# Kernel optimization log

Hardware: AMD Instinct MI355X
Metric: run time of the kernel (lower is better)

## Reference

```python
import jax, jax.numpy as jnp
import numpy as np

B, D, W, H = 512, 128, 256, 256  # batch, drive_num, window_size, hidden_size


def setup_inputs() -> dict:
    key = jax.random.key(0)
    k = jax.random.split(key, 7)
    x = jax.random.normal(k[0], (B, D, W), jnp.float32)
    # encode_attn: Linear(window_size + 2*hidden_size, 1)
    attn_w = jax.random.normal(k[1], (W + 2 * H,), jnp.float32) * 0.02
    attn_b = jax.random.normal(k[2], (), jnp.float32) * 0.02
    # single-layer LSTM, input_size=D, hidden_size=H; PyTorch gate order i,f,g,o
    W_ih = jax.random.normal(k[3], (4 * H, D), jnp.float32) * 0.05
    W_hh = jax.random.normal(k[4], (4 * H, H), jnp.float32) * 0.05
    b_ih = jax.random.normal(k[5], (4 * H,), jnp.float32) * 0.05
    b_hh = jax.random.normal(k[6], (4 * H,), jnp.float32) * 0.05
    return {"x": x, "attn_w": attn_w, "attn_b": attn_b,
            "W_ih": W_ih, "W_hh": W_hh, "b_ih": b_ih, "b_hh": b_hh}


def reference(x, attn_w, attn_b, W_ih, W_hh, b_ih, b_hh):
    # x: [B, D, W]
    h_dim = W_hh.shape[1]
    w_h = attn_w[:h_dim]           # weight on repeated hidden state
    w_c = attn_w[h_dim:2 * h_dim]  # weight on repeated cell state
    w_x = attn_w[2 * h_dim:]       # weight on full input row (constant over t)
    # precompute input contribution to attention logits: [B, D]
    e_x = jnp.einsum('bdw,w->bd', x, w_x) + attn_b
    x_steps = jnp.moveaxis(x, 2, 0)  # [W, B, D]

    def step(carry, x_t):
        h, c = carry  # [B, H] each
        # attention logit: h/c terms broadcast over drive dim
        e = e_x + (h @ w_h + c @ w_c)[:, None]  # [B, D]
        a = jax.nn.softmax(e, axis=-1)
        x_hat = a * x_t  # [B, D]
        gates = x_hat @ W_ih.T + b_ih + h @ W_hh.T + b_hh  # [B, 4H]
        i, f, g, o = jnp.split(gates, 4, axis=-1)
        c_new = jax.nn.sigmoid(f) * c + jax.nn.sigmoid(i) * jnp.tanh(g)
        h_new = jax.nn.sigmoid(o) * jnp.tanh(c_new)
        return (h_new, c_new), h_new

    bsz = x.shape[0]
    h0 = jnp.zeros((bsz, h_dim), x.dtype)
    c0 = jnp.zeros((bsz, h_dim), x.dtype)
    _, hs = jax.lax.scan(step, (h0, c0), x_steps)  # hs: [W, B, H]
    return jnp.transpose(hs, (1, 0, 2))  # [B, W, H] == hidden_states[:, 1:]
```

## Files before the change

kernel.cpp:

```cpp
#include <hip/hip_runtime.h>
#include <cstdint>

#define NB 512
#define ND 128
#define NW 256
#define NH 256
#define PGRP 32
#define QGRP 8

typedef _Float16 f16;
typedef _Float16 h8 __attribute__((ext_vector_type(8)));
typedef float f32x4 __attribute__((ext_vector_type(4)));
typedef unsigned long long u64;

#define FLAG_DONE 0x0101010101010101ull

__device__ __forceinline__ float sigm(float v){ return 1.f/(1.f+__expf(-v)); }
__device__ __forceinline__ float tanh_fast(float v){
  v = fminf(fmaxf(v,-15.f),15.f);
  float e = __expf(2.f*v);
  return (e-1.f)/(e+1.f);
}

__global__ __launch_bounds__(128) void attn_kernel(
    const float* __restrict__ x, const float* __restrict__ attn_w,
    const float* __restrict__ attn_b, float* __restrict__ a_buf)
{
    __shared__ float wx[NW];
    __shared__ float sred[2];
    const int b = blockIdx.x;
    const int d = threadIdx.x;

    wx[d]       = attn_w[2 * NH + d];
    wx[d + 128] = attn_w[2 * NH + d + 128];
    __syncthreads();

    const float4* xr = (const float4*)(x + ((size_t)b * ND + d) * NW);
    float acc = 0.f;
    #pragma unroll 8
    for (int w4 = 0; w4 < NW / 4; ++w4) {
        float4 v = xr[w4];
        acc += v.x * wx[w4*4+0] + v.y * wx[w4*4+1]
             + v.z * wx[w4*4+2] + v.w * wx[w4*4+3];
    }
    float e = acc + attn_b[0];

    float mx = e;
    #pragma unroll
    for (int o = 32; o > 0; o >>= 1) mx = fmaxf(mx, __shfl_xor(mx, o));
    if ((d & 63) == 0) sred[d >> 6] = mx;
    __syncthreads();
    mx = fmaxf(sred[0], sred[1]);
    __syncthreads();

    float p = __expf(e - mx);
    float s = p;
    #pragma unroll
    for (int o = 32; o > 0; o >>= 1) s += __shfl_xor(s, o);
    if ((d & 63) == 0) sred[d >> 6] = s;
    __syncthreads();
    s = sred[0] + sred[1];

    a_buf[(size_t)b * ND + d] = p / s;
}

__global__ __launch_bounds__(512) void pack_kernel(
    const float* __restrict__ W_ih, const float* __restrict__ W_hh,
    const float* __restrict__ b_ih, const float* __restrict__ b_hh,
    f16* __restrict__ Wfrag, float* __restrict__ bias)
{
    int flat = blockIdx.x * 512 + threadIdx.x;
    int l    = flat & 63;
    int kt   = (flat >> 6) % 12;
    int wq   = (flat >> 6) / 12;
    int col16 = l & 15, kb = l >> 4;
    int hcol = (wq >> 3) * 32 + (wq & 7) * 4 + (col16 >> 2);
    int gate = col16 & 3;
    int n    = gate * 256 + hcol;
    int k0   = kt * 32 + kb * 8;

    f16 tmp[8];
    #pragma unroll
    for (int e = 0; e < 8; ++e) {
        int k = k0 + e;
        float v = (k < NH) ? W_hh[(size_t)n * NH + k]
                           : W_ih[(size_t)n * ND + (k - NH)];
        tmp[e] = (f16)v;
    }
    *(h8*)(Wfrag + (size_t)flat * 8) = *(const h8*)tmp;

    if (flat < 1024) bias[flat] = b_ih[flat] + b_hh[flat];
}

__global__ __launch_bounds__(512) void init_kernel(unsigned* __restrict__ flags)
{
    flags[blockIdx.x * 512 + threadIdx.x] = 0u;
}

__global__ __launch_bounds__(512, 2) void lstm_kernel(
    const float* __restrict__ x, const float* __restrict__ a_buf,
    const float* __restrict__ bias, const f16* __restrict__ Wfrag,
    f16* __restrict__ hx, u64* __restrict__ flags,
    float* __restrict__ out)
{
    __shared__ __align__(16) unsigned char A16[16 * 768];
    __shared__ float scr[8][272];

    const int tid = threadIdx.x;
    const int w = tid >> 6, l = tid & 63;
    const int p = blockIdx.x & 31, q = blockIdx.x >> 5;

    h8 bfrag[12];
    {
        const h8* wsrc = (const h8*)Wfrag + ((q * 8 + w) * 12) * 64 + l;
        #pragma unroll
        for (int kt = 0; kt < 12; ++kt) bfrag[kt] = wsrc[kt * 64];
    }

    const int m = l >> 2, hh = l & 3;
    const int jcol = q * 32 + w * 4 + hh;
    float bias4[4];
    #pragma unroll
    for (int g = 0; g < 4; ++g) bias4[g] = bias[g * 256 + jcol];
    float cstate = 0.f;

    float areg[8];
    const float* xbase = nullptr;
    const int xrow = tid >> 4, xdc = tid & 15;
    if (tid < 256) {
        int b = p * 16 + xrow;
        #pragma unroll
        for (int e = 0; e < 8; ++e) areg[e] = a_buf[b * ND + xdc * 8 + e];
        xbase = x + ((size_t)b * ND + xdc * 8) * NW;
    }
    const int r2 = tid >> 5, kc = tid & 31;
    const int arow = l & 15, akb = l >> 4;

    float4 xq[8];

    {
        int byte = r2 * 768 + kc * 16;
        byte ^= (r2 & 7) << 4;
        h8 z = {};
        *(h8*)(A16 + byte) = z;
    }
    if (tid < 256) {
        #pragma unroll
        for (int e = 0; e < 8; ++e)
            xq[e] = *(const float4*)(xbase + (size_t)e * NW);
        f16 xv[8];
        #pragma unroll
        for (int e = 0; e < 8; ++e) {
            float xf = xq[e].x;
            xq[e] = make_float4(xq[e].y, xq[e].z, xq[e].w, xq[e].x);
            xv[e] = (f16)(xf * areg[e]);
        }
        int byte = xrow * 768 + 512 + xdc * 16;
        byte ^= (xrow & 7) << 4;
        *(h8*)(A16 + byte) = *(const h8*)xv;
    }

    for (int t = 0; t < NW; ++t) {
        if (t > 0 && tid == 0) {
            while (__hip_atomic_load(&flags[(t - 1) * PGRP + p],
                                     __ATOMIC_RELAXED, __HIP_MEMORY_SCOPE_AGENT)
                   != FLAG_DONE) {}
        }
        __syncthreads();

        f32x4 acc = {0.f, 0.f, 0.f, 0.f};
        if (t > 0) {
            const u64* hrow = (const u64*)
                (hx + ((size_t)((t - 1) & 1) * NB + p * 16 + r2) * NH);
            u64 d0 = __hip_atomic_load(hrow + kc * 2 + 0,
                    __ATOMIC_RELAXED, __HIP_MEMORY_SCOPE_AGENT);
            u64 d1 = __hip_atomic_load(hrow + kc * 2 + 1,
                    __ATOMIC_RELAXED, __HIP_MEMORY_SCOPE_AGENT);
            #pragma unroll
            for (int kt = 8; kt < 12; ++kt) {
                int byte = arow * 768 + kt * 64 + akb * 16;
                byte ^= (arow & 7) << 4;
                h8 afrag = *(const h8*)(A16 + byte);
                acc = __builtin_amdgcn_mfma_f32_16x16x32_f16(afrag, bfrag[kt], acc, 0, 0, 0);
            }
            int byte = r2 * 768 + kc * 16;
            byte ^= (r2 & 7) << 4;
            ((u64*)(A16 + byte))[0] = d0;
            ((u64*)(A16 + byte))[1] = d1;
        } else {
            #pragma unroll
            for (int kt = 8; kt < 12; ++kt) {
                int byte = arow * 768 + kt * 64 + akb * 16;
                byte ^= (arow & 7) << 4;
                h8 afrag = *(const h8*)(A16 + byte);
                acc = __builtin_amdgcn_mfma_f32_16x16x32_f16(afrag, bfrag[kt], acc, 0, 0, 0);
            }
        }
        __syncthreads();

        #pragma unroll
        for (int kt = 0; kt < 8; ++kt) {
            int byte = arow * 768 + kt * 64 + akb * 16;
            byte ^= (arow & 7) << 4;
            h8 afrag = *(const h8*)(A16 + byte);
            acc = __builtin_amdgcn_mfma_f32_16x16x32_f16(afrag, bfrag[kt], acc, 0, 0, 0);
        }

        float hn;
        {
            float* sw = &scr[w][0];
            int col = l & 15, rb = (l >> 4) * 4;
            sw[(rb + 0) * 17 + col] = acc[0];
            sw[(rb + 1) * 17 + col] = acc[1];
            sw[(rb + 2) * 17 + col] = acc[2];
            sw[(rb + 3) * 17 + col] = acc[3];
            asm volatile("s_waitcnt lgkmcnt(0)" ::: "memory");
            float G0 = sw[m * 17 + hh * 4 + 0] + bias4[0];
            float G1 = sw[m * 17 + hh * 4 + 1] + bias4[1];
            float G2 = sw[m * 17 + hh * 4 + 2] + bias4[2];
            float G3 = sw[m * 17 + hh * 4 + 3] + bias4[3];
            float ig = sigm(G0), fg = sigm(G1);
            float gg = tanh_fast(G2), og = sigm(G3);
            cstate = fg * cstate + ig * gg;
            hn = og * tanh_fast(cstate);

            f16 hf = (f16)hn;
            unsigned short hb = __builtin_bit_cast(unsigned short, hf);
            int other = __shfl_xor((int)hb, 1);
            if (!(l & 1)) {
                unsigned val = (unsigned)hb | ((unsigned)(unsigned short)other << 16);
                unsigned* dst = (unsigned*)((unsigned short*)hx
                                + ((size_t)(t & 1) * NB + p * 16 + m) * NH + jcol);
                __hip_atomic_store(dst, val, __ATOMIC_RELAXED, __HIP_MEMORY_SCOPE_AGENT);
            }
        }
        asm volatile("s_waitcnt vmcnt(0)" ::: "memory");
        __syncthreads();

        if (tid == 0) {
            unsigned char* fb = ((unsigned char*)&flags[t * PGRP + p]) + q;
            __hip_atomic_store(fb, (unsigned char)1,
                               __ATOMIC_RELAXED, __HIP_MEMORY_SCOPE_AGENT);
        }

        out[((size_t)(p * 16 + m) * NW + t) * NH + jcol] = hn;

        if (tid < 256 && t + 1 < NW) {
            if (((t + 1) & 3) == 0) {
                #pragma unroll
                for (int e = 0; e < 8; ++e)
                    xq[e] = *(const float4*)(xbase + (size_t)e * NW + (t + 1));
            }
            f16 xv[8];
            #pragma unroll
            for (int e = 0; e < 8; ++e) {
                float xf = xq[e].x;
                xq[e] = make_float4(xq[e].y, xq[e].z, xq[e].w, xq[e].x);
                xv[e] = (f16)(xf * areg[e]);
            }
            int byte = xrow * 768 + 512 + xdc * 16;
            byte ^= (xrow & 7) << 4;
            *(h8*)(A16 + byte) = *(const h8*)xv;
        }
    }
}

extern "C" void kernel_launch(void* const* d_in, const int* in_sizes, int n_in,
                              void* d_out, int out_size, void* d_ws, size_t ws_size,
                              hipStream_t stream) {
    (void)in_sizes; (void)n_in; (void)out_size;

    const float* x      = (const float*)d_in[0];
    const float* attn_w = (const float*)d_in[1];
    const float* attn_b = (const float*)d_in[2];
    const float* W_ih   = (const float*)d_in[3];
    const float* W_hh   = (const float*)d_in[4];
    const float* b_ih   = (const float*)d_in[5];
    const float* b_hh   = (const float*)d_in[6];
    float* out = (float*)d_out;

    char* ws = (char*)d_ws;
    float* a_buf = (float*)ws;
    float* bias  = (float*)(ws + 262144);
    f16*   Wfrag = (f16*)(ws + 266240);
    f16*   hx    = (f16*)(ws + 1052672);
    u64*   flags = (u64*)(ws + 1576960);
    if (ws_size < (size_t)1642496) return;

    attn_kernel<<<NB, 128, 0, stream>>>(x, attn_w, attn_b, a_buf);
    pack_kernel<<<96, 512, 0, stream>>>(W_ih, W_hh, b_ih, b_hh, Wfrag, bias);
    init_kernel<<<32, 512, 0, stream>>>((unsigned*)flags);
    lstm_kernel<<<PGRP * QGRP, 512, 0, stream>>>(x, a_buf, bias, Wfrag, hx, flags, out);
}
```

Baseline: 797.8 us.

## Replace per-step flag barrier with sentinel-poisoned hidden-state ring buffer polling

Removes the per-timestep flag word and the single-thread spin plus block barrier. Consumers now poll the hidden-state data directly until no fp16 infinity sentinel remains. Producers re-poison a slot three steps ahead in an 8-slot ring, and the x-input MFMAs are issued before the wait. This cuts one global round trip and a barrier from the cross-block dependency chain on each step. In exchange every thread spins on global loads, and correctness depends on the sentinel value never occurring as a real h value (fp16 +inf) and on the slot-reuse distance.

Result: slower. 818.7 us (+2.6%).

```diff
diff --git a/kernel.cpp b/kernel.cpp
--- a/kernel.cpp
+++ b/kernel.cpp
@@ -7,13 +7,14 @@
 #define NH 256
 #define PGRP 32
 #define QGRP 8
+#define SLOTS 8
+#define SENT32 0x7C007C00u
+#define SENT64 0x7C007C007C007C00ull
 
 typedef _Float16 f16;
 typedef _Float16 h8 __attribute__((ext_vector_type(8)));
 typedef float f32x4 __attribute__((ext_vector_type(4)));
 typedef unsigned long long u64;
-
-#define FLAG_DONE 0x0101010101010101ull
 
 __device__ __forceinline__ float sigm(float v){ return 1.f/(1.f+__expf(-v)); }
 __device__ __forceinline__ float tanh_fast(float v){
@@ -92,16 +93,16 @@
     if (flat < 1024) bias[flat] = b_ih[flat] + b_hh[flat];
 }
 
-__global__ __launch_bounds__(512) void init_kernel(unsigned* __restrict__ flags)
-{
-    flags[blockIdx.x * 512 + threadIdx.x] = 0u;
+__global__ __launch_bounds__(512) void poison_kernel(uint4* __restrict__ hx4)
+{
+    uint4 v = {SENT32, SENT32, SENT32, SENT32};
+    hx4[(size_t)blockIdx.x * 512 + threadIdx.x] = v;
 }
 
 __global__ __launch_bounds__(512, 2) void lstm_kernel(
     const float* __restrict__ x, const float* __restrict__ a_buf,
     const float* __restrict__ bias, const f16* __restrict__ Wfrag,
-    f16* __restrict__ hx, u64* __restrict__ flags,
-    float* __restrict__ out)
+    f16* __restrict__ hx, float* __restrict__ out)
 {
     __shared__ __align__(16) unsigned char A16[16 * 768];
     __shared__ float scr[8][272];
@@ -135,6 +136,7 @@
     }
     const int r2 = tid >> 5, kc = tid & 31;
     const int arow = l & 15, akb = l >> 4;
+    const int pr = tid >> 3, pc = tid & 7;
 
     float4 xq[8];
 
@@ -159,42 +161,35 @@
         byte ^= (xrow & 7) << 4;
         *(h8*)(A16 + byte) = *(const h8*)xv;
     }
+    __syncthreads();
 
     for (int t = 0; t < NW; ++t) {
-        if (t > 0 && tid == 0) {
-            while (__hip_atomic_load(&flags[(t - 1) * PGRP + p],
-                                     __ATOMIC_RELAXED, __HIP_MEMORY_SCOPE_AGENT)
-                   != FLAG_DONE) {}
-        }
-        __syncthreads();
-
         f32x4 acc = {0.f, 0.f, 0.f, 0.f};
+        #pragma unroll
+        for (int kt = 8; kt < 12; ++kt) {
+            int byte = arow * 768 + kt * 64 + akb * 16;
+            byte ^= (arow & 7) << 4;
+            h8 afrag = *(const h8*)(A16 + byte);
+            acc = __builtin_amdgcn_mfma_f32_16x16x32_f16(afrag, bfrag[kt], acc, 0, 0, 0);
+        }
+
         if (t > 0) {
             const u64* hrow = (const u64*)
-                (hx + ((size_t)((t - 1) & 1) * NB + p * 16 + r2) * NH);
-            u64 d0 = __hip_atomic_load(hrow + kc * 2 + 0,
-                    __ATOMIC_RELAXED, __HIP_MEMORY_SCOPE_AGENT);
-            u64 d1 = __hip_atomic_load(hrow + kc * 2 + 1,
-                    __ATOMIC_RELAXED, __HIP_MEMORY_SCOPE_AGENT);
-            #pragma unroll
-            for (int kt = 8; kt < 12; ++kt) {
-                int byte = arow * 768 + kt * 64 + akb * 16;
-                byte ^= (arow & 7) << 4;
-                h8 afrag = *(const h8*)(A16 + byte);
-                acc = __builtin_amdgcn_mfma_f32_16x16x32_f16(afrag, bfrag[kt], acc, 0, 0, 0);
+                (hx + ((size_t)((t - 1) & 7) * NB + p * 16 + r2) * NH);
+            u64 d0, d1;
+            for (;;) {
+                d0 = __hip_atomic_load(hrow + kc * 2 + 0,
+                        __ATOMIC_RELAXED, __HIP_MEMORY_SCOPE_AGENT);
+                d1 = __hip_atomic_load(hrow + kc * 2 + 1,
+                        __ATOMIC_RELAXED, __HIP_MEMORY_SCOPE_AGENT);
+                if ((unsigned)d0 != SENT32 && (unsigned)(d0 >> 32) != SENT32 &&
+                    (unsigned)d1 != SENT32 && (unsigned)(d1 >> 32) != SENT32) break;
+                __builtin_amdgcn_s_sleep(1);
             }
             int byte = r2 * 768 + kc * 16;
             byte ^= (r2 & 7) << 4;
             ((u64*)(A16 + byte))[0] = d0;
             ((u64*)(A16 + byte))[1] = d1;
-        } else {
-            #pragma unroll
-            for (int kt = 8; kt < 12; ++kt) {
-                int byte = arow * 768 + kt * 64 + akb * 16;
-                byte ^= (arow & 7) << 4;
-                h8 afrag = *(const h8*)(A16 + byte);
-                acc = __builtin_amdgcn_mfma_f32_16x16x32_f16(afrag, bfrag[kt], acc, 0, 0, 0);
-            }
         }
         __syncthreads();
 
@@ -223,27 +218,29 @@
             float gg = tanh_fast(G2), og = sigm(G3);
             cstate = fg * cstate + ig * gg;
             hn = og * tanh_fast(cstate);
-
+        }
+
+        asm volatile("s_waitcnt vmcnt(0)" ::: "memory");
+
+        {
             f16 hf = (f16)hn;
             unsigned short hb = __builtin_bit_cast(unsigned short, hf);
             int other = __shfl_xor((int)hb, 1);
             if (!(l & 1)) {
                 unsigned val = (unsigned)hb | ((unsigned)(unsigned short)other << 16);
                 unsigned* dst = (unsigned*)((unsigned short*)hx
-                                + ((size_t)(t & 1) * NB + p * 16 + m) * NH + jcol);
+                                + ((size_t)(t & 7) * NB + p * 16 + m) * NH + jcol);
                 __hip_atomic_store(dst, val, __ATOMIC_RELAXED, __HIP_MEMORY_SCOPE_AGENT);
             }
         }
-        asm volatile("s_waitcnt vmcnt(0)" ::: "memory");
-        __syncthreads();
-
-        if (tid == 0) {
-            unsigned char* fb = ((unsigned char*)&flags[t * PGRP + p]) + q;
-            __hip_atomic_store(fb, (unsigned char)1,
-                               __ATOMIC_RELAXED, __HIP_MEMORY_SCOPE_AGENT);
-        }
 
         out[((size_t)(p * 16 + m) * NW + t) * NH + jcol] = hn;
+
+        if (tid < 128) {
+            u64* pb = (u64*)((unsigned short*)hx
+                     + ((size_t)((t + 3) & 7) * NB + p * 16 + pr) * NH + q * 32 + pc * 4);
+            __hip_atomic_store(pb, SENT64, __ATOMIC_RELAXED, __HIP_MEMORY_SCOPE_AGENT);
+        }
 
         if (tid < 256 && t + 1 < NW) {
             if (((t + 1) & 3) == 0) {
@@ -262,6 +259,7 @@
             byte ^= (xrow & 7) << 4;
             *(h8*)(A16 + byte) = *(const h8*)xv;
         }
+        __syncthreads();
     }
 }
 
@@ -284,11 +282,10 @@
     float* bias  = (float*)(ws + 262144);
     f16*   Wfrag = (f16*)(ws + 266240);
     f16*   hx    = (f16*)(ws + 1052672);
-    u64*   flags = (u64*)(ws + 1576960);
-    if (ws_size < (size_t)1642496) return;
+    if (ws_size < (size_t)(1052672 + 2097152)) return;
 
     attn_kernel<<<NB, 128, 0, stream>>>(x, attn_w, attn_b, a_buf);
     pack_kernel<<<96, 512, 0, stream>>>(W_ih, W_hh, b_ih, b_hh, Wfrag, bias);
-    init_kernel<<<32, 512, 0, stream>>>((unsigned*)flags);
-    lstm_kernel<<<PGRP * QGRP, 512, 0, stream>>>(x, a_buf, bias, Wfrag, hx, flags, out);
-}
+    poison_kernel<<<256, 512, 0, stream>>>((uint4*)hx);
+    lstm_kernel<<<PGRP * QGRP, 512, 0, stream>>>(x, a_buf, bias, Wfrag, hx, out);
+}
```
